# Kernel optimization log

Hardware: AMD Instinct MI355X
Metric: run time of the kernel (lower is better)

## Reference

```python
import jax, jax.numpy as jnp
import numpy as np
import math

NUM_HEADS = 16
ROPE_THETA = 10000.0
NEG_INF = 1.0e6  # fill value from masked_softmax in the source


def _rope(x, positions, theta=ROPE_THETA):
    # x: (..., S, d_k), positions: (S,)
    d_k = x.shape[-1]
    pair_idx = jnp.arange(0, d_k, 2, dtype=jnp.float32)
    inv_freq = 1.0 / (theta ** (pair_idx / d_k))            # (d_k/2,)
    angles = positions[:, None].astype(jnp.float32) * inv_freq  # (S, d_k/2)
    cos = jnp.cos(angles).astype(x.dtype)
    sin = jnp.sin(angles).astype(x.dtype)
    x_even = x[..., 0::2]
    x_odd = x[..., 1::2]
    out_even = x_even * cos - x_odd * sin
    out_odd = x_even * sin + x_odd * cos
    return jnp.stack([out_even, out_odd], axis=-1).reshape(x.shape)


def setup_inputs() -> dict:
    key = jax.random.key(0)
    ks = jax.random.split(key, 5)
    B, S, D = 4, 2048, 1024
    scale = 1.0 / math.sqrt(D)
    return {
        "x": jax.random.normal(ks[0], (B, S, D), dtype=jnp.float32),
        "w_q": jax.random.normal(ks[1], (D, D), dtype=jnp.float32) * scale,
        "w_k": jax.random.normal(ks[2], (D, D), dtype=jnp.float32) * scale,
        "w_v": jax.random.normal(ks[3], (D, D), dtype=jnp.float32) * scale,
        "w_o": jax.random.normal(ks[4], (D, D), dtype=jnp.float32) * scale,
    }


def reference(x, w_q, w_k, w_v, w_o):
    B, S, D = x.shape
    H = NUM_HEADS
    d_k = D // H

    def proj(w):
        # Linear: y = x @ W^T, W is (out, in); split heads -> (B, H, S, d_k)
        return jnp.einsum('bsd,ed->bse', x, w).reshape(B, S, H, d_k).transpose(0, 2, 1, 3)

    q = proj(w_q)
    k = proj(w_k)
    v = proj(w_v)

    positions = jnp.arange(S)
    q = _rope(q, positions)
    k = _rope(k, positions)

    scores = jnp.einsum('bhqd,bhkd->bhqk', q, k) / jnp.sqrt(jnp.asarray(d_k, x.dtype))
    causal = jnp.tril(jnp.ones((S, S), dtype=bool))  # allow j <= i
    scores = jnp.where(causal, scores, -NEG_INF)
    attn = jax.nn.softmax(scores, axis=-1)

    out = jnp.einsum('bhqk,bhkd->bhqd', attn, v)        # (B, H, S, d_k)
    out = out.transpose(0, 2, 1, 3).reshape(B, S, D)
    return jnp.einsum('bsd,ed->bse', out, w_o)
```

## Files before the change

### kernel.cpp

```cpp
#include <hip/hip_runtime.h>
#include <math.h>

#define B_  4
#define S_  2048
#define D_  1024
#define H_  16
#define DK_ 64

typedef unsigned short u16;
typedef unsigned int   u32;
typedef short     shortx8  __attribute__((ext_vector_type(8)));
typedef short     short4v  __attribute__((ext_vector_type(4)));
typedef float     floatx4  __attribute__((ext_vector_type(4)));
typedef float     floatx16 __attribute__((ext_vector_type(16)));
typedef u16       u16x4    __attribute__((ext_vector_type(4)));

__device__ __forceinline__ u16 f2bf(float f) {
    u32 u = __float_as_uint(f);
    u += 0x7FFFu + ((u >> 16) & 1u);
    return (u16)(u >> 16);
}
__device__ __forceinline__ float bf2f(u16 b) {
    return __uint_as_float(((u32)b) << 16);
}

typedef const __attribute__((address_space(1))) u32* gp1_t;
typedef __attribute__((address_space(3))) u32* lp3_t;
__device__ __forceinline__ void async16(const void* g, void* l) {
    __builtin_amdgcn_global_load_lds((gp1_t)g, (lp3_t)l, 16, 0, 0);
}

#define MFMA32(a, b, c) __builtin_amdgcn_mfma_f32_16x16x32_bf16((a), (b), (c), 0, 0, 0)
#define MFMA16(a, b, c) __builtin_amdgcn_mfma_f32_32x32x16_bf16((a), (b), (c), 0, 0, 0)
#define MFMA8(a, b, c)  __builtin_amdgcn_mfma_f32_32x32x8bf16_1k((a), (b), (c), 0, 0, 0)

__global__ __launch_bounds__(256)
void split_bf16(const float* __restrict__ src, u16* __restrict__ dh,
                u16* __restrict__ dl, int n)
{
    int i = (blockIdx.x * 256 + threadIdx.x) * 4;
    if (i >= n) return;
    float4 v = *(const float4*)(src + i);
    u16 h0 = f2bf(v.x), h1 = f2bf(v.y), h2 = f2bf(v.z), h3 = f2bf(v.w);
    u16x4 hv = {h0, h1, h2, h3};
    u16x4 lv = {f2bf(v.x - bf2f(h0)), f2bf(v.y - bf2f(h1)),
                f2bf(v.z - bf2f(h2)), f2bf(v.w - bf2f(h3))};
    *(u16x4*)(dh + i) = hv;
    *(u16x4*)(dl + i) = lv;
}

__global__ __launch_bounds__(256)
void fill_rope(float2* __restrict__ tab)
{
    const int idx = blockIdx.x * 256 + threadIdx.x;
    const int s = idx >> 5, i = idx & 31;
    const float fr = powf(10000.0f, -(float)i * (1.0f / 32.0f));
    float sa, ca;
    sincosf((float)s * fr, &sa, &ca);
    tab[idx] = make_float2(ca, sa);
}

template<int EPI>
__global__ __launch_bounds__(256, 1)
void gemm_b3(const u16* __restrict__ Ah, const u16* __restrict__ Al,
             const u16* __restrict__ Wh, const u16* __restrict__ Wl,
             float* __restrict__ outF,
             u16* __restrict__ qoh, u16* __restrict__ qol,
             u16* __restrict__ koh, u16* __restrict__ kol,
             u16* __restrict__ voh,
             const float2* __restrict__ rope,
             int M, int N, int K)
{
    __shared__ __align__(16) u16 As[2][128][32];
    __shared__ __align__(16) u16 Ws[2][128][32];

    const int tid  = threadIdx.x;
    const int w    = tid >> 6;
    const int lane = tid & 63;
    const int lr   = lane & 15, lg = lane >> 4;
    const int wm   = w >> 1, wn = w & 1;

    const int cpx = gridDim.x >> 3;
    const int id  = blockIdx.x;
    const int swz = (id & 7) * cpx + (id >> 3);
    const int m0  = (swz & 63) * 128, n0 = (swz >> 6) * 128;

    const int srow = w * 32 + (lane >> 2);
    const int sck  = (lane & 3) * 8;
    const u16* gAh = Ah + (size_t)(m0 + srow) * K + sck;
    const u16* gAl = Al + (size_t)(m0 + srow) * K + sck;
    const u16* gWh = Wh + (size_t)(n0 + srow) * K + sck;
    const u16* gWl = Wl + (size_t)(n0 + srow) * K + sck;
    const size_t r16 = (size_t)16 * K;

    u16* dAh = &As[0][w * 32][0];
    u16* dAl = &As[1][w * 32][0];
    u16* dWh = &Ws[0][w * 32][0];
    u16* dWl = &Ws[1][w * 32][0];

    floatx4 zero = {0.f, 0.f, 0.f, 0.f};
    floatx4 acc[4][4];
    #pragma unroll
    for (int i = 0; i < 4; ++i)
        #pragma unroll
        for (int j = 0; j < 4; ++j) acc[i][j] = zero;

    for (int kt = 0; kt < K; kt += 32) {
        __syncthreads();
        async16(gAh + kt,       dAh);
        async16(gAh + kt + r16, dAh + 512);
        async16(gAl + kt,       dAl);
        async16(gAl + kt + r16, dAl + 512);
        async16(gWh + kt,       dWh);
        async16(gWh + kt + r16, dWh + 512);
        async16(gWl + kt,       dWl);
        async16(gWl + kt + r16, dWl + 512);
        __syncthreads();

        shortx8 bw0[4], bw1[4];
        #pragma unroll
        for (int ni = 0; ni < 4; ++ni) {
            bw0[ni] = *(const shortx8*)&Ws[0][wn * 64 + ni * 16 + lr][lg * 8];
            bw1[ni] = *(const shortx8*)&Ws[1][wn * 64 + ni * 16 + lr][lg * 8];
        }
        #pragma unroll
        for (int mi = 0; mi < 4; ++mi) {
            shortx8 a0 = *(const shortx8*)&As[0][wm * 64 + mi * 16 + lr][lg * 8];
            shortx8 a1 = *(const shortx8*)&As[1][wm * 64 + mi * 16 + lr][lg * 8];
            #pragma unroll
            for (int ni = 0; ni < 4; ++ni) {
                acc[mi][ni] = MFMA32(a0, bw0[ni], acc[mi][ni]);
                acc[mi][ni] = MFMA32(a0, bw1[ni], acc[mi][ni]);
                acc[mi][ni] = MFMA32(a1, bw0[ni], acc[mi][ni]);
            }
        }
    }

    if constexpr (EPI == 0) {
        #pragma unroll
        for (int mi = 0; mi < 4; ++mi)
            #pragma unroll
            for (int ni = 0; ni < 4; ++ni)
                #pragma unroll
                for (int r = 0; r < 4; ++r) {
                    size_t row = m0 + wm * 64 + mi * 16 + lg * 4 + r;
                    size_t col = n0 + wn * 64 + ni * 16 + lr;
                    outF[row * D_ + col] = acc[mi][ni][r];
                }
    }
    if constexpr (EPI == 3) {
        const int sel = n0 >> 10;
        const int ln0 = n0 & 1023;
        if (sel <= 1) {
            const float scale = (sel == 0) ? 0.125f : 1.0f;
            u16* oh = (sel == 0) ? qoh : koh;
            u16* ol = (sel == 0) ? qol : kol;
            #pragma unroll
            for (int ni = 0; ni < 4; ++ni) {
                const int pi = (ni * 16 + lr) >> 1;
                #pragma unroll
                for (int mi = 0; mi < 4; ++mi)
                    #pragma unroll
                    for (int r = 0; r < 4; ++r) {
                        int row  = m0 + wm * 64 + mi * 16 + lg * 4 + r;
                        float2 cs = rope[((row & (S_ - 1)) << 5) + pi];
                        float v  = acc[mi][ni][r];
                        float pv = __shfl_xor(v, 1);
                        float o  = (v * cs.x + ((lr & 1) ? pv * cs.y : -pv * cs.y)) * scale;
                        u16 hv = f2bf(o);
                        u16 lv = f2bf(o - bf2f(hv));
                        u32 ph  = (u32)__shfl_xor((int)hv, 1) & 0xFFFFu;
                        u32 pl2 = (u32)__shfl_xor((int)lv, 1) & 0xFFFFu;
                        if (!(lr & 1)) {
                            size_t off = (size_t)row * D_ + ln0 + wn * 64 + ni * 16 + lr;
                            *(u32*)(oh + off) = (u32)hv | (ph << 16);
                            *(u32*)(ol + off) = (u32)lv | (pl2 << 16);
                        }
                    }
            }
        } else {
            #pragma unroll
            for (int mi = 0; mi < 4; ++mi)
                #pragma unroll
                for (int ni = 0; ni < 4; ++ni)
                    #pragma unroll
                    for (int r = 0; r < 4; ++r) {
                        float v = acc[mi][ni][r];
                        u16 hv = f2bf(v);
                        u32 ph = (u32)__shfl_xor((int)hv, 1) & 0xFFFFu;
                        if (!(lr & 1)) {
                            size_t row = m0 + wm * 64 + mi * 16 + lg * 4 + r;
                            size_t off = row * D_ + ln0 + wn * 64 + ni * 16 + lr;
                            *(u32*)(voh + off) = (u32)hv | (ph << 16);
                        }
                    }
        }
    }
}

__global__ __launch_bounds__(256)
void attn_mfma(const u16* __restrict__ Qh, const u16* __restrict__ Ql,
               const u16* __restrict__ Kh, const u16* __restrict__ Kl,
               const u16* __restrict__ Vh,
               u16* __restrict__ Oh, u16* __restrict__ Ol)
{
    __shared__ __align__(16) u16 Ksh[64][72];
    __shared__ __align__(16) u16 Ksl[64][72];
    __shared__ __align__(16) u16 Vt[64][68];

    const int tid  = threadIdx.x, w = tid >> 6, lane = tid & 63;
    const int l31  = lane & 31, hi = lane >> 5;
    const int qt   = gridDim.x - 1 - blockIdx.x;
    const int h    = blockIdx.y, b = blockIdx.z;
    const int q0   = qt * 128;
    const size_t rowbase = (size_t)b * S_;
    const int qg   = q0 + w * 32 + l31;

    shortx8 qfh[4], qfl[4];
    {
        const u16* qp  = Qh + (rowbase + qg) * D_ + h * DK_ + hi * 8;
        const u16* qp2 = Ql + (rowbase + qg) * D_ + h * DK_ + hi * 8;
        #pragma unroll
        for (int c = 0; c < 4; ++c) {
            qfh[c] = *(const shortx8*)(qp  + c * 16);
            qfl[c] = *(const shortx8*)(qp2 + c * 16);
        }
    }

    const int kr = tid >> 2, kc = (tid & 3) * 16;
    const u16* gKh = Kh + (rowbase + kr) * D_ + h * DK_ + kc;
    const u16* gKl = Kl + (rowbase + kr) * D_ + h * DK_ + kc;
    const u16* gV  = Vh + (rowbase + lane) * D_ + h * DK_ + w * 16;

    shortx8 rkh[2], rkl[2], rv[2];
    rkh[0] = *(const shortx8*)(gKh);   rkh[1] = *(const shortx8*)(gKh + 8);
    rkl[0] = *(const shortx8*)(gKl);   rkl[1] = *(const shortx8*)(gKl + 8);
    rv[0]  = *(const shortx8*)(gV);    rv[1]  = *(const shortx8*)(gV + 8);

    float mrow = -1e30f, lsum = 0.0f;
    floatx16 oacc[2] = {};

    const int nkt = 2 * qt + 2;
    for (int kt = 0; kt < nkt; ++kt) {
        __syncthreads();
        *(shortx8*)&Ksh[kr][kc]     = rkh[0];
        *(shortx8*)&Ksh[kr][kc + 8] = rkh[1];
        *(shortx8*)&Ksl[kr][kc]     = rkl[0];
        *(shortx8*)&Ksl[kr][kc + 8] = rkl[1];
        #pragma unroll
        for (int j = 0; j < 8; ++j) {
            Vt[w * 16 + j][lane]     = (u16)rv[0][j];
            Vt[w * 16 + 8 + j][lane] = (u16)rv[1][j];
        }
        __syncthreads();

        if (kt < nkt - 1) {
            gKh += (size_t)64 * D_; gKl += (size_t)64 * D_; gV += (size_t)64 * D_;
            rkh[0] = *(const shortx8*)(gKh);   rkh[1] = *(const shortx8*)(gKh + 8);
            rkl[0] = *(const shortx8*)(gKl);   rkl[1] = *(const shortx8*)(gKl + 8);
            rv[0]  = *(const shortx8*)(gV);    rv[1]  = *(const shortx8*)(gV + 8);
        }

        floatx16 sc[2] = {};
        __builtin_amdgcn_s_setprio(1);
        #pragma unroll
        for (int kf = 0; kf < 2; ++kf)
            #pragma unroll
            for (int c = 0; c < 4; ++c) {
                shortx8 ah = *(const shortx8*)&Ksh[kf * 32 + l31][c * 16 + hi * 8];
                shortx8 al = *(const shortx8*)&Ksl[kf * 32 + l31][c * 16 + hi * 8];
                sc[kf] = MFMA16(ah, qfh[c], sc[kf]);
                sc[kf] = MFMA16(al, qfh[c], sc[kf]);
                sc[kf] = MFMA16(ah, qfl[c], sc[kf]);
            }
        __builtin_amdgcn_s_setprio(0);

        const int k0 = kt * 64;
        if (kt >= 2 * qt) {
            #pragma unroll
            for (int kf = 0; kf < 2; ++kf)
                #pragma unroll
                for (int r = 0; r < 16; ++r) {
                    int key = k0 + kf * 32 + (r & 3) + 8 * (r >> 2) + 4 * hi;
                    if (key > qg) sc[kf][r] = -1e30f;
                }
        }

        float t0 = -1e30f, t1 = -1e30f, t2 = -1e30f, t3 = -1e30f;
        #pragma unroll
        for (int kf = 0; kf < 2; ++kf)
            #pragma unroll
            for (int r = 0; r < 16; r += 4) {
                t0 = fmaxf(t0, sc[kf][r + 0]);
                t1 = fmaxf(t1, sc[kf][r + 1]);
                t2 = fmaxf(t2, sc[kf][r + 2]);
                t3 = fmaxf(t3, sc[kf][r + 3]);
            }
        float pm = fmaxf(fmaxf(t0, t1), fmaxf(t2, t3));
        pm = fmaxf(pm, __shfl_xor(pm, 32));
        const float mn   = fmaxf(mrow, pm);
        const float corr = __expf(mrow - mn);
        mrow = mn;
        float s0 = 0.f, s1 = 0.f, s2 = 0.f, s3 = 0.f;
        #pragma unroll
        for (int kf = 0; kf < 2; ++kf)
            #pragma unroll
            for (int r = 0; r < 16; r += 4) {
                s0 += (sc[kf][r + 0] = __expf(sc[kf][r + 0] - mn));
                s1 += (sc[kf][r + 1] = __expf(sc[kf][r + 1] - mn));
                s2 += (sc[kf][r + 2] = __expf(sc[kf][r + 2] - mn));
                s3 += (sc[kf][r + 3] = __expf(sc[kf][r + 3] - mn));
            }
        float ls = (s0 + s1) + (s2 + s3);
        ls += __shfl_xor(ls, 32);
        lsum = lsum * corr + ls;
        oacc[0] *= corr;
        oacc[1] *= corr;

        short4v pb[8];
        #pragma unroll
        for (int kc2 = 0; kc2 < 8; ++kc2)
            #pragma unroll
            for (int j = 0; j < 4; ++j)
                pb[kc2][j] = (short)f2bf(sc[kc2 >> 2][(kc2 & 3) * 4 + j]);

        __builtin_amdgcn_s_setprio(1);
        #pragma unroll
        for (int kc2 = 0; kc2 < 8; ++kc2) {
            short4v va0 = *(const short4v*)&Vt[l31][kc2 * 8 + hi * 4];
            short4v va1 = *(const short4v*)&Vt[32 + l31][kc2 * 8 + hi * 4];
            oacc[0] = MFMA8(va0, pb[kc2], oacc[0]);
            oacc[1] = MFMA8(va1, pb[kc2], oacc[1]);
        }
        __builtin_amdgcn_s_setprio(0);
    }

    const float inv = 1.0f / lsum;
    #pragma unroll
    for (int df = 0; df < 2; ++df)
        #pragma unroll
        for (int rp = 0; rp < 8; ++rp) {
            const int r0 = rp * 2;
            const int d  = df * 32 + (r0 & 3) + 8 * (r0 >> 2) + 4 * hi;
            float v0 = oacc[df][r0] * inv;
            float v1 = oacc[df][r0 + 1] * inv;
            u16 h0 = f2bf(v0), h1 = f2bf(v1);
            u16 e0 = f2bf(v0 - bf2f(h0)), e1 = f2bf(v1 - bf2f(h1));
            size_t off = (rowbase + qg) * D_ + h * DK_ + d;
            *(u32*)(Oh + off) = (u32)h0 | ((u32)h1 << 16);
            *(u32*)(Ol + off) = (u32)e0 | ((u32)e1 << 16);
        }
}

extern "C" void kernel_launch(void* const* d_in, const int* in_sizes, int n_in,
                              void* d_out, int out_size, void* d_ws, size_t ws_size,
                              hipStream_t stream)
{
    const float* x   = (const float*)d_in[0];
    const float* w_q = (const float*)d_in[1];
    const float* w_k = (const float*)d_in[2];
    const float* w_v = (const float*)d_in[3];
    const float* w_o = (const float*)d_in[4];
    float* out = (float*)d_out;

    const size_t TEN = (size_t)B_ * S_ * D_;
    const int    DD  = D_ * D_;
    const int    M   = B_ * S_;

    u16* p    = (u16*)d_ws;
    u16* xh   = p;             u16* xl   = xh + TEN;
    u16* qh   = xl + TEN;      u16* ql   = qh + TEN;
    u16* kh   = ql + TEN;      u16* kl   = kh + TEN;
    u16* vh   = kl + TEN;
    u16* wch  = vh + TEN;
    u16* wcl  = wch + (size_t)3 * DD;
    u16* woh  = wcl + (size_t)3 * DD;
    u16* wol  = woh + DD;
    float2* rope = (float2*)(wol + DD);

    split_bf16<<<(int)(TEN / 1024), 256, 0, stream>>>(x, xh, xl, (int)TEN);
    split_bf16<<<DD / 1024, 256, 0, stream>>>(w_q, wch,          wcl,          DD);
    split_bf16<<<DD / 1024, 256, 0, stream>>>(w_k, wch + DD,     wcl + DD,     DD);
    split_bf16<<<DD / 1024, 256, 0, stream>>>(w_v, wch + 2 * DD, wcl + 2 * DD, DD);
    split_bf16<<<DD / 1024, 256, 0, stream>>>(w_o, woh, wol, DD);
    fill_rope<<<256, 256, 0, stream>>>(rope);

    gemm_b3<3><<<dim3((M / 128) * (3 * D_ / 128)), 256, 0, stream>>>(
        xh, xl, wch, wcl, nullptr, qh, ql, kh, kl, vh, rope, M, 3 * D_, D_);

    attn_mfma<<<dim3(S_ / 128, H_, B_), 256, 0, stream>>>(qh, ql, kh, kl, vh,
                                                          qh, ql);

    gemm_b3<0><<<dim3((M / 128) * (D_ / 128)), 256, 0, stream>>>(
        qh, ql, woh, wol, out, nullptr, nullptr, nullptr, nullptr, nullptr,
        nullptr, M, D_, D_);
}
```

Baseline: 544.2 us.

## Double-buffer LDS tiles in split-bf16 GEMM to overlap loads with MFMA

```diff
diff --git a/kernel.cpp b/kernel.cpp
--- a/kernel.cpp
+++ b/kernel.cpp
@@ -71,8 +71,8 @@
              const float2* __restrict__ rope,
              int M, int N, int K)
 {
-    __shared__ __align__(16) u16 As[2][128][32];
-    __shared__ __align__(16) u16 Ws[2][128][32];
+    __shared__ __align__(16) u16 As[2][2][128][32];
+    __shared__ __align__(16) u16 Ws[2][2][128][32];
 
     const int tid  = threadIdx.x;
     const int w    = tid >> 6;
@@ -85,18 +85,22 @@
     const int swz = (id & 7) * cpx + (id >> 3);
     const int m0  = (swz & 63) * 128, n0 = (swz >> 6) * 128;
 
-    const int srow = w * 32 + (lane >> 2);
-    const int sck  = (lane & 3) * 8;
-    const u16* gAh = Ah + (size_t)(m0 + srow) * K + sck;
-    const u16* gAl = Al + (size_t)(m0 + srow) * K + sck;
-    const u16* gWh = Wh + (size_t)(n0 + srow) * K + sck;
-    const u16* gWl = Wl + (size_t)(n0 + srow) * K + sck;
+    const u16* gAh = Ah + (size_t)(m0 + w * 32 + (lane >> 2)) * K + (lane & 3) * 8;
+    const u16* gAl = Al + (size_t)(m0 + w * 32 + (lane >> 2)) * K + (lane & 3) * 8;
+    const u16* gWh = Wh + (size_t)(n0 + w * 32 + (lane >> 2)) * K + (lane & 3) * 8;
+    const u16* gWl = Wl + (size_t)(n0 + w * 32 + (lane >> 2)) * K + (lane & 3) * 8;
     const size_t r16 = (size_t)16 * K;
 
-    u16* dAh = &As[0][w * 32][0];
-    u16* dAl = &As[1][w * 32][0];
-    u16* dWh = &Ws[0][w * 32][0];
-    u16* dWl = &Ws[1][w * 32][0];
+    auto STAGE = [&](int buf, int kt) {
+        async16(gAh + kt,       &As[buf][0][w * 32][0]);
+        async16(gAh + kt + r16, &As[buf][0][w * 32 + 16][0]);
+        async16(gAl + kt,       &As[buf][1][w * 32][0]);
+        async16(gAl + kt + r16, &As[buf][1][w * 32 + 16][0]);
+        async16(gWh + kt,       &Ws[buf][0][w * 32][0]);
+        async16(gWh + kt + r16, &Ws[buf][0][w * 32 + 16][0]);
+        async16(gWl + kt,       &Ws[buf][1][w * 32][0]);
+        async16(gWl + kt + r16, &Ws[buf][1][w * 32 + 16][0]);
+    };
 
     floatx4 zero = {0.f, 0.f, 0.f, 0.f};
     floatx4 acc[4][4];
@@ -105,35 +109,28 @@
         #pragma unroll
         for (int j = 0; j < 4; ++j) acc[i][j] = zero;
 
+    STAGE(0, 0);
+    int cur = 0;
     for (int kt = 0; kt < K; kt += 32) {
         __syncthreads();
-        async16(gAh + kt,       dAh);
-        async16(gAh + kt + r16, dAh + 512);
-        async16(gAl + kt,       dAl);
-        async16(gAl + kt + r16, dAl + 512);
-        async16(gWh + kt,       dWh);
-        async16(gWh + kt + r16, dWh + 512);
-        async16(gWl + kt,       dWl);
-        async16(gWl + kt + r16, dWl + 512);
-        __syncthreads();
-
-        shortx8 bw0[4], bw1[4];
-        #pragma unroll
-        for (int ni = 0; ni < 4; ++ni) {
-            bw0[ni] = *(const shortx8*)&Ws[0][wn * 64 + ni * 16 + lr][lg * 8];
-            bw1[ni] = *(const shortx8*)&Ws[1][wn * 64 + ni * 16 + lr][lg * 8];
-        }
-        #pragma unroll
-        for (int mi = 0; mi < 4; ++mi) {
-            shortx8 a0 = *(const shortx8*)&As[0][wm * 64 + mi * 16 + lr][lg * 8];
-            shortx8 a1 = *(const shortx8*)&As[1][wm * 64 + mi * 16 + lr][lg * 8];
+        shortx8 a0[4], a1[4], bw0[4], bw1[4];
+        #pragma unroll
+        for (int i = 0; i < 4; ++i) {
+            a0[i]  = *(const shortx8*)&As[cur][0][wm * 64 + i * 16 + lr][lg * 8];
+            a1[i]  = *(const shortx8*)&As[cur][1][wm * 64 + i * 16 + lr][lg * 8];
+            bw0[i] = *(const shortx8*)&Ws[cur][0][wn * 64 + i * 16 + lr][lg * 8];
+            bw1[i] = *(const shortx8*)&Ws[cur][1][wn * 64 + i * 16 + lr][lg * 8];
+        }
+        if (kt + 32 < K) STAGE(cur ^ 1, kt + 32);
+        #pragma unroll
+        for (int mi = 0; mi < 4; ++mi)
             #pragma unroll
             for (int ni = 0; ni < 4; ++ni) {
-                acc[mi][ni] = MFMA32(a0, bw0[ni], acc[mi][ni]);
-                acc[mi][ni] = MFMA32(a0, bw1[ni], acc[mi][ni]);
-                acc[mi][ni] = MFMA32(a1, bw0[ni], acc[mi][ni]);
-            }
-        }
+                acc[mi][ni] = MFMA32(a0[mi], bw0[ni], acc[mi][ni]);
+                acc[mi][ni] = MFMA32(a0[mi], bw1[ni], acc[mi][ni]);
+                acc[mi][ni] = MFMA32(a1[mi], bw0[ni], acc[mi][ni]);
+            }
+        cur ^= 1;
     }
 
     if constexpr (EPI == 0) {
```

Measured after the change: 532.5 us. 2.1% less time.
